# Kernel tuning notes

Hardware: AMD Instinct MI355X
Metric: run time of the kernel (lower is better)

Reference implementation:

```python
import jax, jax.numpy as jnp
import numpy as np

LN_EPS = 1e-5

def _mlp(h, W1, b1, g1, beta1, W2, b2):
    # Linear -> LayerNorm -> SiLU -> Linear (make_mlp with 2 layers, output_activation=None)
    h = h @ W1 + b1
    mu = h.mean(-1, keepdims=True)
    var = h.var(-1, keepdims=True)  # biased var, matches torch LayerNorm
    h = (h - mu) * jax.lax.rsqrt(var + LN_EPS) * g1 + beta1
    h = jax.nn.silu(h)
    return h @ W2 + b2

def setup_inputs() -> dict:
    key = jax.random.key(0)
    ks = jax.random.split(key, 8)
    N, E, H = 50000, 800000, 128
    def init_w(k, fan_in, fan_out):
        lim = 1.0 / np.sqrt(fan_in)
        return jax.random.uniform(k, (fan_in, fan_out), jnp.float32, -lim, lim)
    return {
        "x": jax.random.normal(ks[0], (N, H), jnp.float32),
        "edge_index": jax.random.randint(ks[1], (2, E), 0, N),
        "e": jax.random.normal(ks[2], (E, H), jnp.float32),
        # node network: in 2H (cat of x and sum-aggregated messages)
        "Wn1": init_w(ks[3], 2 * H, H), "bn1": jnp.zeros((H,), jnp.float32),
        "gn1": jnp.ones((H,), jnp.float32), "betan1": jnp.zeros((H,), jnp.float32),
        "Wn2": init_w(ks[4], H, H), "bn2": jnp.zeros((H,), jnp.float32),
        # edge network: in 3H (cat of x_out[start], x_out[end], e)
        "We1": init_w(ks[5], 3 * H, H), "be1": jnp.zeros((H,), jnp.float32),
        "ge1": jnp.ones((H,), jnp.float32), "betae1": jnp.zeros((H,), jnp.float32),
        "We2": init_w(ks[6], H, H), "be2": jnp.zeros((H,), jnp.float32),
    }

def reference(x, edge_index, e, Wn1, bn1, gn1, betan1, Wn2, bn2, We1, be1, ge1, betae1, We2, be2):
    start, end = edge_index[0], edge_index[1]
    # aggregation == 'sum': scatter_add of edge features onto destination nodes
    msgs = jax.ops.segment_sum(e, end, num_segments=x.shape[0])  # [N, H]
    node_inputs = jnp.concatenate([x, msgs], axis=-1)  # [N, 2H]
    x_out = _mlp(node_inputs, Wn1, bn1, gn1, betan1, Wn2, bn2) + x  # residual
    edge_inputs = jnp.concatenate([x_out[start], x_out[end], e], axis=-1)  # [E, 3H]
    e_out = _mlp(edge_inputs, We1, be1, ge1, betae1, We2, be2) + e  # residual
    return (x_out, e_out)
```

## Files before the change

### kernel.cpp

```cpp
#include <hip/hip_runtime.h>

#define H 128
#define LN_EPS 1e-5f

typedef __attribute__((ext_vector_type(8))) short bf16x8;
typedef __attribute__((ext_vector_type(4))) float f32x4;

__device__ __forceinline__ ushort f2bf(float f) {
    unsigned u = __builtin_bit_cast(unsigned, f);
    u += 0x7fffu + ((u >> 16) & 1u);
    return (ushort)(u >> 16);
}

__device__ __forceinline__ f32x4 mfma16(bf16x8 a, bf16x8 b, f32x4 c) {
    return __builtin_amdgcn_mfma_f32_16x16x32_bf16(a, b, c, 0, 0, 0);
}

__global__ __launch_bounds__(256) void hist_kernel(
    const int* __restrict__ ei, int* __restrict__ cnt, int E)
{
    int i = blockIdx.x * 256 + threadIdx.x;
    if (i < E) atomicAdd(&cnt[ei[E + i]], 1);
}

__global__ __launch_bounds__(1024) void scan_kernel(
    const int* __restrict__ cnt, int* __restrict__ off, int N)
{
    __shared__ int s[1024];
    const int t = threadIdx.x;
    const int chunk = (N + 1023) / 1024;
    const int lo = t * chunk, hi = min(lo + chunk, N);
    int sum = 0;
    for (int i = lo; i < hi; ++i) sum += cnt[i];
    s[t] = sum;
    __syncthreads();
    for (int d = 1; d < 1024; d <<= 1) {
        int v = (t >= d) ? s[t - d] : 0;
        __syncthreads();
        s[t] += v;
        __syncthreads();
    }
    int running = s[t] - sum;
    for (int i = lo; i < hi; ++i) {
        off[i] = running;
        running += cnt[i];
    }
    if (t == 1023) off[N] = running;
}

__global__ __launch_bounds__(256) void reorder_kernel(
    const int* __restrict__ ei, int* __restrict__ cursor,
    int* __restrict__ sorted, int E)
{
    int i = blockIdx.x * 256 + threadIdx.x;
    if (i < E) {
        int pos = atomicAdd(&cursor[ei[E + i]], 1);
        sorted[pos] = i;
    }
}

__global__ __launch_bounds__(256) void segsum_kernel(
    const float* __restrict__ e, const int* __restrict__ sorted,
    const int* __restrict__ off, float* __restrict__ msgs, int N)
{
    int node = blockIdx.x * 4 + (threadIdx.x >> 6);
    int lane = threadIdx.x & 63;
    if (node >= N) return;
    int beg = off[node], end = off[node + 1];
    float ax = 0.f, ay = 0.f;
    for (int base = beg; base < end; base += 64) {
        int eid_l = (base + lane < end) ? sorted[base + lane] : 0;
        int cnt = min(64, end - base);
        int i = 0;
        for (; i + 4 <= cnt; i += 4) {
            int e0 = __shfl(eid_l, i), e1 = __shfl(eid_l, i + 1);
            int e2 = __shfl(eid_l, i + 2), e3 = __shfl(eid_l, i + 3);
            float2 v0 = *reinterpret_cast<const float2*>(e + (size_t)e0 * H + lane * 2);
            float2 v1 = *reinterpret_cast<const float2*>(e + (size_t)e1 * H + lane * 2);
            float2 v2 = *reinterpret_cast<const float2*>(e + (size_t)e2 * H + lane * 2);
            float2 v3 = *reinterpret_cast<const float2*>(e + (size_t)e3 * H + lane * 2);
            ax += v0.x + v1.x + v2.x + v3.x;
            ay += v0.y + v1.y + v2.y + v3.y;
        }
        for (; i < cnt; ++i) {
            int eid = __shfl(eid_l, i);
            float2 v = *reinterpret_cast<const float2*>(e + (size_t)eid * H + lane * 2);
            ax += v.x; ay += v.y;
        }
    }
    *reinterpret_cast<float2*>(msgs + (size_t)node * H + lane * 2) = make_float2(ax, ay);
}

__global__ __launch_bounds__(256) void wtrans_kernel(
    const float* __restrict__ W, ushort* __restrict__ Wt, int K)
{
    int idx = blockIdx.x * 256 + threadIdx.x;
    if (idx >= K * H) return;
    int k = idx >> 7, n = idx & (H - 1);
    Wt[n * K + k] = f2bf(W[idx]);
}

__global__ __launch_bounds__(256, 4) void node_mlp_kernel(
    const float* __restrict__ x, const float* __restrict__ msgs,
    const ushort* __restrict__ W1t, const float* __restrict__ b1,
    const float* __restrict__ g1, const float* __restrict__ be1,
    const ushort* __restrict__ W2t, const float* __restrict__ b2,
    float* __restrict__ x_out, ushort* __restrict__ xbf, int N)
{
    __shared__ ushort smem[64 * 264];
    __shared__ float part_s[2][64], part_q[2][64];

    const int tid = threadIdx.x;
    const int row0 = blockIdx.x * 64;

    for (int idx = tid; idx < 64 * 64; idx += 256) {
        int r = idx >> 6, c4 = idx & 63;
        int row = row0 + r;
        float4 v = make_float4(0.f, 0.f, 0.f, 0.f);
        if (row < N)
            v = (c4 < 32) ? reinterpret_cast<const float4*>(x + (size_t)row * H)[c4]
                          : reinterpret_cast<const float4*>(msgs + (size_t)row * H)[c4 - 32];
        ushort4 bv;
        bv.x = f2bf(v.x); bv.y = f2bf(v.y); bv.z = f2bf(v.z); bv.w = f2bf(v.w);
        *reinterpret_cast<ushort4*>(&smem[r * 264 + c4 * 4]) = bv;
    }
    __syncthreads();

    const int lane = tid & 63, w = tid >> 6;
    const int l15 = lane & 15, lg = lane >> 4;
    const int mrow = (w & 1) * 32, ncol = (w >> 1) * 64;

    const ushort* pi0 = smem + (size_t)(mrow + l15) * 264;
    const ushort* pi1 = smem + (size_t)(mrow + 16 + l15) * 264;
    const ushort* pw1 = W1t + (size_t)(ncol + l15) * 256;

    f32x4 acc[2][4];
    #pragma unroll
    for (int mt = 0; mt < 2; ++mt)
        #pragma unroll
        for (int nt = 0; nt < 4; ++nt)
            acc[mt][nt] = (f32x4){0.f, 0.f, 0.f, 0.f};

    #pragma unroll
    for (int ks = 0; ks < 8; ++ks) {
        int k0 = ks * 32 + lg * 8;
        bf16x8 a0 = *reinterpret_cast<const bf16x8*>(pi0 + k0);
        bf16x8 a1 = *reinterpret_cast<const bf16x8*>(pi1 + k0);
        #pragma unroll
        for (int nt = 0; nt < 4; ++nt) {
            bf16x8 bfr = *reinterpret_cast<const bf16x8*>(pw1 + (size_t)nt * 16 * 256 + k0);
            acc[0][nt] = mfma16(a0, bfr, acc[0][nt]);
            acc[1][nt] = mfma16(a1, bfr, acc[1][nt]);
        }
    }

    float b1c[4], g1c[4], be1c[4];
    #pragma unroll
    for (int nt = 0; nt < 4; ++nt) {
        int c = ncol + nt * 16 + l15;
        b1c[nt] = b1[c]; g1c[nt] = g1[c]; be1c[nt] = be1[c];
    }
    #pragma unroll
    for (int mt = 0; mt < 2; ++mt)
        #pragma unroll
        for (int nt = 0; nt < 4; ++nt)
            #pragma unroll
            for (int r = 0; r < 4; ++r)
                acc[mt][nt][r] += b1c[nt];

    #pragma unroll
    for (int mt = 0; mt < 2; ++mt) {
        #pragma unroll
        for (int r = 0; r < 4; ++r) {
            float s = acc[mt][0][r] + acc[mt][1][r] + acc[mt][2][r] + acc[mt][3][r];
            float q = acc[mt][0][r] * acc[mt][0][r] + acc[mt][1][r] * acc[mt][1][r]
                    + acc[mt][2][r] * acc[mt][2][r] + acc[mt][3][r] * acc[mt][3][r];
            #pragma unroll
            for (int m = 8; m >= 1; m >>= 1) {
                s += __shfl_xor(s, m);
                q += __shfl_xor(q, m);
            }
            if (l15 == 0) {
                int rl = mrow + mt * 16 + lg * 4 + r;
                part_s[w >> 1][rl] = s;
                part_q[w >> 1][rl] = q;
            }
        }
    }
    __syncthreads();

    #pragma unroll
    for (int mt = 0; mt < 2; ++mt) {
        #pragma unroll
        for (int r = 0; r < 4; ++r) {
            int rl = mrow + mt * 16 + lg * 4 + r;
            float s  = part_s[0][rl] + part_s[1][rl];
            float q  = part_q[0][rl] + part_q[1][rl];
            float mu = s * (1.0f / H);
            float rs = rsqrtf(q * (1.0f / H) - mu * mu + LN_EPS);
            #pragma unroll
            for (int nt = 0; nt < 4; ++nt) {
                float v = (acc[mt][nt][r] - mu) * rs * g1c[nt] + be1c[nt];
                v = v / (1.0f + __expf(-v));
                smem[rl * 136 + ncol + nt * 16 + l15] = f2bf(v);
            }
        }
    }
    __syncthreads();

    const ushort* ph0 = smem + (size_t)(mrow + l15) * 136;
    const ushort* ph1 = smem + (size_t)(mrow + 16 + l15) * 136;
    const ushort* pw2 = W2t + (size_t)(ncol + l15) * 128;

    f32x4 acc2[2][4];
    #pragma unroll
    for (int nt = 0; nt < 4; ++nt) {
        float bb = b2[ncol + nt * 16 + l15];
        #pragma unroll
        for (int mt = 0; mt < 2; ++mt)
            acc2[mt][nt] = (f32x4){bb, bb, bb, bb};
    }
    #pragma unroll
    for (int ks = 0; ks < 4; ++ks) {
        int k0 = ks * 32 + lg * 8;
        bf16x8 a0 = *reinterpret_cast<const bf16x8*>(ph0 + k0);
        bf16x8 a1 = *reinterpret_cast<const bf16x8*>(ph1 + k0);
        #pragma unroll
        for (int nt = 0; nt < 4; ++nt) {
            bf16x8 bfr = *reinterpret_cast<const bf16x8*>(pw2 + (size_t)nt * 16 * 128 + k0);
            acc2[0][nt] = mfma16(a0, bfr, acc2[0][nt]);
            acc2[1][nt] = mfma16(a1, bfr, acc2[1][nt]);
        }
    }

    #pragma unroll
    for (int mt = 0; mt < 2; ++mt) {
        #pragma unroll
        for (int r = 0; r < 4; ++r) {
            int row = row0 + mrow + mt * 16 + lg * 4 + r;
            if (row < N) {
                const float* rp = x + (size_t)row * H;
                float* op = x_out + (size_t)row * H;
                ushort* bp = xbf + (size_t)row * H;
                #pragma unroll
                for (int nt = 0; nt < 4; ++nt) {
                    int c = ncol + nt * 16 + l15;
                    float o = acc2[mt][nt][r] + rp[c];
                    op[c] = o;
                    bp[c] = f2bf(o);
                }
            }
        }
    }
}

__global__ __launch_bounds__(256, 4) void edge_mlp_kernel(
    const ushort* __restrict__ xbf, const float* __restrict__ e,
    const int* __restrict__ ei,
    const ushort* __restrict__ W1t, const float* __restrict__ b1,
    const float* __restrict__ g1, const float* __restrict__ be1,
    const ushort* __restrict__ W2t, const float* __restrict__ b2,
    float* __restrict__ e_out, int E)
{
    __shared__ ushort smem[64 * 136];
    __shared__ float part_s[2][64], part_q[2][64];
    __shared__ int sidx[64], eidx[64];

    const int tid = threadIdx.x;
    const int row0 = blockIdx.x * 64;

    if (tid < 64) {
        int row = row0 + tid;
        sidx[tid] = (row < E) ? ei[row] : 0;
        eidx[tid] = (row < E) ? ei[E + row] : 0;
    }

    for (int idx = tid; idx < 64 * 32; idx += 256) {
        int r = idx >> 5, c4 = idx & 31;
        int row = row0 + r;
        float4 v = make_float4(0.f, 0.f, 0.f, 0.f);
        if (row < E)
            v = reinterpret_cast<const float4*>(e + (size_t)row * H)[c4];
        ushort4 bv;
        bv.x = f2bf(v.x); bv.y = f2bf(v.y); bv.z = f2bf(v.z); bv.w = f2bf(v.w);
        *reinterpret_cast<ushort4*>(&smem[r * 136 + c4 * 4]) = bv;
    }
    __syncthreads();

    const int lane = tid & 63, w = tid >> 6;
    const int l15 = lane & 15, lg = lane >> 4;
    const int mrow = (w & 1) * 32, ncol = (w >> 1) * 64;
    const int rA0 = mrow + l15, rA1 = mrow + 16 + l15;

    const ushort* ps0 = xbf + (size_t)sidx[rA0] * H + lg * 8;
    const ushort* ps1 = xbf + (size_t)sidx[rA1] * H + lg * 8;
    const ushort* pd0 = xbf + (size_t)eidx[rA0] * H + lg * 8;
    const ushort* pd1 = xbf + (size_t)eidx[rA1] * H + lg * 8;

    bf16x8 axs0[4], axs1[4], axd0[4], axd1[4];
    #pragma unroll
    for (int k = 0; k < 4; ++k) {
        axs0[k] = *reinterpret_cast<const bf16x8*>(ps0 + k * 32);
        axs1[k] = *reinterpret_cast<const bf16x8*>(ps1 + k * 32);
        axd0[k] = *reinterpret_cast<const bf16x8*>(pd0 + k * 32);
        axd1[k] = *reinterpret_cast<const bf16x8*>(pd1 + k * 32);
    }

    const ushort* pe0 = smem + (size_t)rA0 * 136 + lg * 8;
    const ushort* pe1 = smem + (size_t)rA1 * 136 + lg * 8;
    const ushort* pw1 = W1t + (size_t)(ncol + l15) * 384 + lg * 8;

    f32x4 acc[2][4];
    #pragma unroll
    for (int mt = 0; mt < 2; ++mt)
        #pragma unroll
        for (int nt = 0; nt < 4; ++nt)
            acc[mt][nt] = (f32x4){0.f, 0.f, 0.f, 0.f};

    #pragma unroll
    for (int ks = 0; ks < 12; ++ks) {
        bf16x8 a0, a1;
        if (ks < 4)      { a0 = axs0[ks];     a1 = axs1[ks];     }
        else if (ks < 8) { a0 = axd0[ks - 4]; a1 = axd1[ks - 4]; }
        else {
            a0 = *reinterpret_cast<const bf16x8*>(pe0 + (ks - 8) * 32);
            a1 = *reinterpret_cast<const bf16x8*>(pe1 + (ks - 8) * 32);
        }
        #pragma unroll
        for (int nt = 0; nt < 4; ++nt) {
            bf16x8 bfr = *reinterpret_cast<const bf16x8*>(pw1 + (size_t)nt * 16 * 384 + ks * 32);
            acc[0][nt] = mfma16(a0, bfr, acc[0][nt]);
            acc[1][nt] = mfma16(a1, bfr, acc[1][nt]);
        }
    }

    float b1c[4], g1c[4], be1c[4];
    #pragma unroll
    for (int nt = 0; nt < 4; ++nt) {
        int c = ncol + nt * 16 + l15;
        b1c[nt] = b1[c]; g1c[nt] = g1[c]; be1c[nt] = be1[c];
    }
    #pragma unroll
    for (int mt = 0; mt < 2; ++mt)
        #pragma unroll
        for (int nt = 0; nt < 4; ++nt)
            #pragma unroll
            for (int r = 0; r < 4; ++r)
                acc[mt][nt][r] += b1c[nt];

    #pragma unroll
    for (int mt = 0; mt < 2; ++mt) {
        #pragma unroll
        for (int r = 0; r < 4; ++r) {
            float s = acc[mt][0][r] + acc[mt][1][r] + acc[mt][2][r] + acc[mt][3][r];
            float q = acc[mt][0][r] * acc[mt][0][r] + acc[mt][1][r] * acc[mt][1][r]
                    + acc[mt][2][r] * acc[mt][2][r] + acc[mt][3][r] * acc[mt][3][r];
            #pragma unroll
            for (int m = 8; m >= 1; m >>= 1) {
                s += __shfl_xor(s, m);
                q += __shfl_xor(q, m);
            }
            if (l15 == 0) {
                int rl = mrow + mt * 16 + lg * 4 + r;
                part_s[w >> 1][rl] = s;
                part_q[w >> 1][rl] = q;
            }
        }
    }
    __syncthreads();

    #pragma unroll
    for (int mt = 0; mt < 2; ++mt) {
        #pragma unroll
        for (int r = 0; r < 4; ++r) {
            int rl = mrow + mt * 16 + lg * 4 + r;
            float s  = part_s[0][rl] + part_s[1][rl];
            float q  = part_q[0][rl] + part_q[1][rl];
            float mu = s * (1.0f / H);
            float rs = rsqrtf(q * (1.0f / H) - mu * mu + LN_EPS);
            #pragma unroll
            for (int nt = 0; nt < 4; ++nt) {
                float v = (acc[mt][nt][r] - mu) * rs * g1c[nt] + be1c[nt];
                v = v / (1.0f + __expf(-v));
                smem[rl * 136 + ncol + nt * 16 + l15] = f2bf(v);
            }
        }
    }
    __syncthreads();

    const ushort* ph0 = smem + (size_t)rA0 * 136;
    const ushort* ph1 = smem + (size_t)rA1 * 136;
    const ushort* pw2 = W2t + (size_t)(ncol + l15) * 128;

    f32x4 acc2[2][4];
    #pragma unroll
    for (int nt = 0; nt < 4; ++nt) {
        float bb = b2[ncol + nt * 16 + l15];
        #pragma unroll
        for (int mt = 0; mt < 2; ++mt)
            acc2[mt][nt] = (f32x4){bb, bb, bb, bb};
    }
    #pragma unroll
    for (int ks = 0; ks < 4; ++ks) {
        int k0 = ks * 32 + lg * 8;
        bf16x8 a0 = *reinterpret_cast<const bf16x8*>(ph0 + k0);
        bf16x8 a1 = *reinterpret_cast<const bf16x8*>(ph1 + k0);
        #pragma unroll
        for (int nt = 0; nt < 4; ++nt) {
            bf16x8 bfr = *reinterpret_cast<const bf16x8*>(pw2 + (size_t)nt * 16 * 128 + k0);
            acc2[0][nt] = mfma16(a0, bfr, acc2[0][nt]);
            acc2[1][nt] = mfma16(a1, bfr, acc2[1][nt]);
        }
    }

    #pragma unroll
    for (int mt = 0; mt < 2; ++mt) {
        #pragma unroll
        for (int r = 0; r < 4; ++r) {
            int row = row0 + mrow + mt * 16 + lg * 4 + r;
            if (row < E) {
                const float* rp = e + (size_t)row * H;
                float* op = e_out + (size_t)row * H;
                #pragma unroll
                for (int nt = 0; nt < 4; ++nt) {
                    int c = ncol + nt * 16 + l15;
                    op[c] = acc2[mt][nt][r] + rp[c];
                }
            }
        }
    }
}

extern "C" void kernel_launch(void* const* d_in, const int* in_sizes, int n_in,
                              void* d_out, int out_size, void* d_ws, size_t ws_size,
                              hipStream_t stream)
{
    const float* x     = (const float*)d_in[0];
    const int*   ei    = (const int*)  d_in[1];
    const float* e     = (const float*)d_in[2];
    const float* Wn1   = (const float*)d_in[3];
    const float* bn1   = (const float*)d_in[4];
    const float* gn1   = (const float*)d_in[5];
    const float* betan1= (const float*)d_in[6];
    const float* Wn2   = (const float*)d_in[7];
    const float* bn2   = (const float*)d_in[8];
    const float* We1   = (const float*)d_in[9];
    const float* be1   = (const float*)d_in[10];
    const float* ge1   = (const float*)d_in[11];
    const float* betae1= (const float*)d_in[12];
    const float* We2   = (const float*)d_in[13];
    const float* be2   = (const float*)d_in[14];

    const int N = in_sizes[0] / H;
    const int E = in_sizes[2] / H;

    float* x_out = (float*)d_out;
    float* e_out = (float*)d_out + (long long)N * H;

    char* p = (char*)d_ws;
    float*  msgs = (float*)p;            p += (size_t)N * H * sizeof(float);
    ushort* xbf  = (ushort*)p;           p += (size_t)N * H * sizeof(ushort);
    ushort* Wn1t = (ushort*)p;           p += (size_t)256 * H * sizeof(ushort);
    ushort* Wn2t = (ushort*)p;           p += (size_t)H * H * sizeof(ushort);
    ushort* We1t = (ushort*)p;           p += (size_t)384 * H * sizeof(ushort);
    ushort* We2t = (ushort*)p;           p += (size_t)H * H * sizeof(ushort);
    p = (char*)(((size_t)p + 15) & ~(size_t)15);
    int* cnt    = (int*)p;               p += (size_t)N * sizeof(int);
    int* off    = (int*)p;               p += ((size_t)N + 1) * sizeof(int);
    int* cursor = (int*)p;               p += (size_t)N * sizeof(int);
    int* sorted = (int*)p;               p += (size_t)E * sizeof(int);

    wtrans_kernel<<<(256 * H + 255) / 256, 256, 0, stream>>>(Wn1, Wn1t, 256);
    wtrans_kernel<<<(H * H + 255) / 256, 256, 0, stream>>>(Wn2, Wn2t, H);
    wtrans_kernel<<<(384 * H + 255) / 256, 256, 0, stream>>>(We1, We1t, 384);
    wtrans_kernel<<<(H * H + 255) / 256, 256, 0, stream>>>(We2, We2t, H);

    hipMemsetAsync(cnt, 0, (size_t)N * sizeof(int), stream);
    hist_kernel<<<(E + 255) / 256, 256, 0, stream>>>(ei, cnt, E);
    scan_kernel<<<1, 1024, 0, stream>>>(cnt, off, N);
    hipMemcpyAsync(cursor, off, (size_t)N * sizeof(int),
                   hipMemcpyDeviceToDevice, stream);
    reorder_kernel<<<(E + 255) / 256, 256, 0, stream>>>(ei, cursor, sorted, E);
    segsum_kernel<<<(N + 3) / 4, 256, 0, stream>>>(e, sorted, off, msgs, N);

    {
        int blocks = (N + 63) / 64;
        node_mlp_kernel<<<blocks, 256, 0, stream>>>(
            x, msgs, Wn1t, bn1, gn1, betan1, Wn2t, bn2, x_out, xbf, N);
    }
    {
        int blocks = (E + 63) / 64;
        edge_mlp_kernel<<<blocks, 256, 0, stream>>>(
            xbf, e, ei, We1t, be1, ge1, betae1, We2t, be2, e_out, E);
    }
}
```

Baseline: 864.8 us.

## Load edge features directly into registers in edge MLP, drop LDS staging

The edge MLP kernel no longer stages e and the edge indices through shared memory with a block barrier. Each lane now loads its own rows of e straight into registers, converts them with packed bf16 instructions, and splits the loads so the second half overlaps the first MFMA phases. The occupancy hint drops from 4 to 3 to make room for the extra live registers. Separately, the scan kernel now writes the cursor array itself, removing a device-to-device memcpy.

```diff
diff --git a/kernel.cpp b/kernel.cpp
--- a/kernel.cpp
+++ b/kernel.cpp
@@ -12,6 +12,15 @@
     return (ushort)(u >> 16);
 }
 
+__device__ __forceinline__ bf16x8 cvt8(float4 lo, float4 hi) {
+    union { bf16x8 v; unsigned u[4]; } r;
+    asm("v_cvt_pk_bf16_f32 %0, %1, %2" : "=v"(r.u[0]) : "v"(lo.x), "v"(lo.y));
+    asm("v_cvt_pk_bf16_f32 %0, %1, %2" : "=v"(r.u[1]) : "v"(lo.z), "v"(lo.w));
+    asm("v_cvt_pk_bf16_f32 %0, %1, %2" : "=v"(r.u[2]) : "v"(hi.x), "v"(hi.y));
+    asm("v_cvt_pk_bf16_f32 %0, %1, %2" : "=v"(r.u[3]) : "v"(hi.z), "v"(hi.w));
+    return r.v;
+}
+
 __device__ __forceinline__ f32x4 mfma16(bf16x8 a, bf16x8 b, f32x4 c) {
     return __builtin_amdgcn_mfma_f32_16x16x32_bf16(a, b, c, 0, 0, 0);
 }
@@ -24,7 +33,8 @@
 }
 
 __global__ __launch_bounds__(1024) void scan_kernel(
-    const int* __restrict__ cnt, int* __restrict__ off, int N)
+    const int* __restrict__ cnt, int* __restrict__ off,
+    int* __restrict__ cursor, int N)
 {
     __shared__ int s[1024];
     const int t = threadIdx.x;
@@ -43,6 +53,7 @@
     int running = s[t] - sum;
     for (int i = lo; i < hi; ++i) {
         off[i] = running;
+        cursor[i] = running;
         running += cnt[i];
     }
     if (t == 1023) off[N] = running;
@@ -254,7 +265,7 @@
     }
 }
 
-__global__ __launch_bounds__(256, 4) void edge_mlp_kernel(
+__global__ __launch_bounds__(256, 3) void edge_mlp_kernel(
     const ushort* __restrict__ xbf, const float* __restrict__ e,
     const int* __restrict__ ei,
     const ushort* __restrict__ W1t, const float* __restrict__ b1,
@@ -262,52 +273,46 @@
     const ushort* __restrict__ W2t, const float* __restrict__ b2,
     float* __restrict__ e_out, int E)
 {
-    __shared__ ushort smem[64 * 136];
+    __shared__ ushort h_s[64 * 136];
     __shared__ float part_s[2][64], part_q[2][64];
-    __shared__ int sidx[64], eidx[64];
 
     const int tid = threadIdx.x;
     const int row0 = blockIdx.x * 64;
-
-    if (tid < 64) {
-        int row = row0 + tid;
-        sidx[tid] = (row < E) ? ei[row] : 0;
-        eidx[tid] = (row < E) ? ei[E + row] : 0;
-    }
-
-    for (int idx = tid; idx < 64 * 32; idx += 256) {
-        int r = idx >> 5, c4 = idx & 31;
-        int row = row0 + r;
-        float4 v = make_float4(0.f, 0.f, 0.f, 0.f);
-        if (row < E)
-            v = reinterpret_cast<const float4*>(e + (size_t)row * H)[c4];
-        ushort4 bv;
-        bv.x = f2bf(v.x); bv.y = f2bf(v.y); bv.z = f2bf(v.z); bv.w = f2bf(v.w);
-        *reinterpret_cast<ushort4*>(&smem[r * 136 + c4 * 4]) = bv;
-    }
-    __syncthreads();
-
     const int lane = tid & 63, w = tid >> 6;
     const int l15 = lane & 15, lg = lane >> 4;
     const int mrow = (w & 1) * 32, ncol = (w >> 1) * 64;
     const int rA0 = mrow + l15, rA1 = mrow + 16 + l15;
-
-    const ushort* ps0 = xbf + (size_t)sidx[rA0] * H + lg * 8;
-    const ushort* ps1 = xbf + (size_t)sidx[rA1] * H + lg * 8;
-    const ushort* pd0 = xbf + (size_t)eidx[rA0] * H + lg * 8;
-    const ushort* pd1 = xbf + (size_t)eidx[rA1] * H + lg * 8;
-
-    bf16x8 axs0[4], axs1[4], axd0[4], axd1[4];
-    #pragma unroll
-    for (int k = 0; k < 4; ++k) {
-        axs0[k] = *reinterpret_cast<const bf16x8*>(ps0 + k * 32);
-        axs1[k] = *reinterpret_cast<const bf16x8*>(ps1 + k * 32);
-        axd0[k] = *reinterpret_cast<const bf16x8*>(pd0 + k * 32);
-        axd1[k] = *reinterpret_cast<const bf16x8*>(pd1 + k * 32);
-    }
-
-    const ushort* pe0 = smem + (size_t)rA0 * 136 + lg * 8;
-    const ushort* pe1 = smem + (size_t)rA1 * 136 + lg * 8;
+    const int gr0 = min(row0 + rA0, E - 1);
+    const int gr1 = min(row0 + rA1, E - 1);
+
+    const int s0 = ei[gr0], s1 = ei[gr1];
+    const int d0 = ei[E + gr0], d1 = ei[E + gr1];
+
+    const ushort* ps0 = xbf + (size_t)s0 * H + lg * 8;
+    const ushort* ps1 = xbf + (size_t)s1 * H + lg * 8;
+    const ushort* pd0 = xbf + (size_t)d0 * H + lg * 8;
+    const ushort* pd1 = xbf + (size_t)d1 * H + lg * 8;
+    const float*  qe0 = e + (size_t)gr0 * H + lg * 8;
+    const float*  qe1 = e + (size_t)gr1 * H + lg * 8;
+
+    bf16x8 xs0[4], xs1[4], xd0[4], xd1[4];
+    #pragma unroll
+    for (int t = 0; t < 4; ++t) {
+        xs0[t] = *reinterpret_cast<const bf16x8*>(ps0 + t * 32);
+        xs1[t] = *reinterpret_cast<const bf16x8*>(ps1 + t * 32);
+        xd0[t] = *reinterpret_cast<const bf16x8*>(pd0 + t * 32);
+        xd1[t] = *reinterpret_cast<const bf16x8*>(pd1 + t * 32);
+    }
+    float4 e0a[2], e0b[2], e1a[2], e1b[2];
+    #pragma unroll
+    for (int t = 0; t < 2; ++t) {
+        e0a[t] = *reinterpret_cast<const float4*>(qe0 + t * 32);
+        e0b[t] = *reinterpret_cast<const float4*>(qe0 + t * 32 + 4);
+        e1a[t] = *reinterpret_cast<const float4*>(qe1 + t * 32);
+        e1b[t] = *reinterpret_cast<const float4*>(qe1 + t * 32 + 4);
+    }
+    __builtin_amdgcn_sched_barrier(0);
+
     const ushort* pw1 = W1t + (size_t)(ncol + l15) * 384 + lg * 8;
 
     f32x4 acc[2][4];
@@ -318,17 +323,52 @@
             acc[mt][nt] = (f32x4){0.f, 0.f, 0.f, 0.f};
 
     #pragma unroll
-    for (int ks = 0; ks < 12; ++ks) {
-        bf16x8 a0, a1;
-        if (ks < 4)      { a0 = axs0[ks];     a1 = axs1[ks];     }
-        else if (ks < 8) { a0 = axd0[ks - 4]; a1 = axd1[ks - 4]; }
-        else {
-            a0 = *reinterpret_cast<const bf16x8*>(pe0 + (ks - 8) * 32);
-            a1 = *reinterpret_cast<const bf16x8*>(pe1 + (ks - 8) * 32);
-        }
-        #pragma unroll
-        for (int nt = 0; nt < 4; ++nt) {
-            bf16x8 bfr = *reinterpret_cast<const bf16x8*>(pw1 + (size_t)nt * 16 * 384 + ks * 32);
+    for (int t = 0; t < 4; ++t) {
+        #pragma unroll
+        for (int nt = 0; nt < 4; ++nt) {
+            bf16x8 bfr = *reinterpret_cast<const bf16x8*>(pw1 + (size_t)nt * 16 * 384 + t * 32);
+            acc[0][nt] = mfma16(xs0[t], bfr, acc[0][nt]);
+            acc[1][nt] = mfma16(xs1[t], bfr, acc[1][nt]);
+        }
+    }
+
+    float4 e0a2[2], e0b2[2], e1a2[2], e1b2[2];
+    #pragma unroll
+    for (int t = 0; t < 2; ++t) {
+        e0a2[t] = *reinterpret_cast<const float4*>(qe0 + (t + 2) * 32);
+        e0b2[t] = *reinterpret_cast<const float4*>(qe0 + (t + 2) * 32 + 4);
+        e1a2[t] = *reinterpret_cast<const float4*>(qe1 + (t + 2) * 32);
+        e1b2[t] = *reinterpret_cast<const float4*>(qe1 + (t + 2) * 32 + 4);
+    }
+
+    #pragma unroll
+    for (int t = 0; t < 4; ++t) {
+        #pragma unroll
+        for (int nt = 0; nt < 4; ++nt) {
+            bf16x8 bfr = *reinterpret_cast<const bf16x8*>(pw1 + (size_t)nt * 16 * 384 + (4 + t) * 32);
+            acc[0][nt] = mfma16(xd0[t], bfr, acc[0][nt]);
+            acc[1][nt] = mfma16(xd1[t], bfr, acc[1][nt]);
+        }
+    }
+
+    #pragma unroll
+    for (int t = 0; t < 2; ++t) {
+        bf16x8 a0 = cvt8(e0a[t], e0b[t]);
+        bf16x8 a1 = cvt8(e1a[t], e1b[t]);
+        #pragma unroll
+        for (int nt = 0; nt < 4; ++nt) {
+            bf16x8 bfr = *reinterpret_cast<const bf16x8*>(pw1 + (size_t)nt * 16 * 384 + (8 + t) * 32);
+            acc[0][nt] = mfma16(a0, bfr, acc[0][nt]);
+            acc[1][nt] = mfma16(a1, bfr, acc[1][nt]);
+        }
+    }
+    #pragma unroll
+    for (int t = 0; t < 2; ++t) {
+        bf16x8 a0 = cvt8(e0a2[t], e0b2[t]);
+        bf16x8 a1 = cvt8(e1a2[t], e1b2[t]);
+        #pragma unroll
+        for (int nt = 0; nt < 4; ++nt) {
+            bf16x8 bfr = *reinterpret_cast<const bf16x8*>(pw1 + (size_t)nt * 16 * 384 + (10 + t) * 32);
             acc[0][nt] = mfma16(a0, bfr, acc[0][nt]);
             acc[1][nt] = mfma16(a1, bfr, acc[1][nt]);
         }
@@ -382,14 +422,14 @@
             for (int nt = 0; nt < 4; ++nt) {
                 float v = (acc[mt][nt][r] - mu) * rs * g1c[nt] + be1c[nt];
                 v = v / (1.0f + __expf(-v));
-                smem[rl * 136 + ncol + nt * 16 + l15] = f2bf(v);
+                h_s[rl * 136 + ncol + nt * 16 + l15] = f2bf(v);
             }
         }
     }
     __syncthreads();
 
-    const ushort* ph0 = smem + (size_t)rA0 * 136;
-    const ushort* ph1 = smem + (size_t)rA1 * 136;
+    const ushort* ph0 = h_s + (size_t)rA0 * 136;
+    const ushort* ph1 = h_s + (size_t)rA1 * 136;
     const ushort* pw2 = W2t + (size_t)(ncol + l15) * 128;
 
     f32x4 acc2[2][4];
@@ -477,9 +517,7 @@
 
     hipMemsetAsync(cnt, 0, (size_t)N * sizeof(int), stream);
     hist_kernel<<<(E + 255) / 256, 256, 0, stream>>>(ei, cnt, E);
-    scan_kernel<<<1, 1024, 0, stream>>>(cnt, off, N);
-    hipMemcpyAsync(cursor, off, (size_t)N * sizeof(int),
-                   hipMemcpyDeviceToDevice, stream);
+    scan_kernel<<<1, 1024, 0, stream>>>(cnt, off, cursor, N);
     reorder_kernel<<<(E + 255) / 256, 256, 0, stream>>>(ei, cursor, sorted, E);
     segsum_kernel<<<(N + 3) / 4, 256, 0, stream>>>(e, sorted, off, msgs, N);
 
```

After: 945.9 us. 9.4% more time.
